# Optimization experiments

Measured on AMD Instinct MI355X. Metric: run time of the kernel, lower is better.

The kernel has to match this reference:

```python
import jax, jax.numpy as jnp
import numpy as np

C = 256
CQK = C // 8  # query/key channel dim from Conv3d(in, in//8, 1)


def setup_inputs() -> dict:
    key = jax.random.key(0)
    ks = jax.random.split(key, 8)
    B, D, H, W = 2, 16, 16, 16
    x = jax.random.normal(ks[0], (B, C, D, H, W), dtype=jnp.float32)
    s = 1.0 / np.sqrt(C)
    q_w = jax.random.normal(ks[1], (CQK, C), dtype=jnp.float32) * s
    q_b = jax.random.normal(ks[2], (CQK,), dtype=jnp.float32) * 0.01
    k_w = jax.random.normal(ks[3], (CQK, C), dtype=jnp.float32) * s
    k_b = jax.random.normal(ks[4], (CQK,), dtype=jnp.float32) * 0.01
    v_w = jax.random.normal(ks[5], (C, C), dtype=jnp.float32) * s
    v_b = jax.random.normal(ks[6], (C,), dtype=jnp.float32) * 0.01
    gamma = jax.random.normal(ks[7], (1,), dtype=jnp.float32)
    return {"x": x, "q_w": q_w, "q_b": q_b, "k_w": k_w, "k_b": k_b,
            "v_w": v_w, "v_b": v_b, "gamma": gamma}


def reference(x, q_w, q_b, k_w, k_b, v_w, v_b, gamma):
    B, Cc, D, H, W = x.shape
    N = D * H * W
    xf = x.reshape(B, Cc, N)  # [B, C, N]
    # 1x1x1 Conv3d == channel-mixing matmul
    q = jnp.einsum('oc,bcn->bon', q_w, xf) + q_b[None, :, None]  # [B, C/8, N]
    k = jnp.einsum('oc,bcn->bon', k_w, xf) + k_b[None, :, None]  # [B, C/8, N]
    v = jnp.einsum('oc,bcn->bon', v_w, xf) + v_b[None, :, None]  # [B, C, N]
    # attention[b, i, j] = sum_c q[b, c, i] * k[b, c, j]
    attn = jnp.einsum('bci,bcj->bij', q, k)  # [B, N, N]
    attn = jax.nn.softmax(attn, axis=-1)
    # out[b, c, i] = sum_j v[b, c, j] * attn[b, i, j]
    out = jnp.einsum('bcj,bij->bci', v, attn)  # [B, C, N]
    out = out.reshape(B, Cc, D, H, W)
    return gamma[0] * out + x
```

## Files before the change

kernel.cpp:

```cpp
#include <hip/hip_runtime.h>

#define C_DIM 256
#define CQK   32
#define N_DIM 4096
#define B_DIM 2

typedef __attribute__((ext_vector_type(8))) short bf16x8;
typedef __attribute__((ext_vector_type(4))) float f32x4;

__device__ __forceinline__ unsigned short f2bf(float f) {
    union { float f; unsigned u; } v; v.f = f;
    unsigned r = v.u + 0x7FFFu + ((v.u >> 16) & 1u);
    return (unsigned short)(r >> 16);
}
__device__ __forceinline__ unsigned pk2(float a, float b) {
    return (unsigned)f2bf(a) | ((unsigned)f2bf(b) << 16);
}
__device__ __forceinline__ unsigned pk2t(float a, float b) {
    union { float f; unsigned u; } ua, ub; ua.f = a; ub.f = b;
    return __builtin_amdgcn_perm(ub.u, ua.u, 0x07060302u);
}
#define EXP2(x) __builtin_amdgcn_exp2f(x)
#define MFMA(A, B, C) __builtin_amdgcn_mfma_f32_16x16x32_bf16((A), (B), (C), 0, 0, 0)

__global__ __launch_bounds__(256) void wconv(
    const float* __restrict__ q_w, const float* __restrict__ q_b,
    const float* __restrict__ k_w, const float* __restrict__ k_b,
    const float* __restrict__ v_w, const float* __restrict__ v_b,
    unsigned short* __restrict__ wbf, float* __restrict__ biasf)
{
    const float LOG2E = 1.4426950408889634f;
    int o = blockIdx.x, c = threadIdx.x;
    float w;
    if (o < 32)       w = q_w[o * C_DIM + c] * LOG2E;
    else if (o < 64)  w = k_w[(o - 32) * C_DIM + c];
    else              w = v_w[(o - 64) * C_DIM + c];
    wbf[o * C_DIM + c] = f2bf(w);
    if (c == 0) biasf[o] = (o < 32) ? q_b[o] * LOG2E
                         : (o < 64) ? k_b[o - 32] : v_b[o - 64];
}

__global__ __launch_bounds__(256, 2) void qkv_proj(
    const float* __restrict__ x, const unsigned short* __restrict__ wbf,
    const float* __restrict__ biasf,
    unsigned short* __restrict__ qT, unsigned short* __restrict__ kT,
    unsigned short* __restrict__ vbf)
{
    __shared__ __align__(16) unsigned short xsT[32 * 264];
    __shared__ __align__(16) unsigned short qkbuf[2][32 * 36];
    __shared__ __align__(16) unsigned short vbb[256 * 36];
    const int t  = threadIdx.x;
    const int b  = blockIdx.x >> 7;
    const int n0 = (blockIdx.x & 127) * 32;

    {
        int n4 = t & 3, cq = t >> 2;
        const float* xp = x + ((size_t)(b * C_DIM + cq * 4)) * N_DIM + n0 + n4 * 8;
        float a0[8], a1[8], a2[8], a3[8];
        *(float4*)(a0)     = *(const float4*)(xp);
        *(float4*)(a0 + 4) = *(const float4*)(xp + 4);
        *(float4*)(a1)     = *(const float4*)(xp + N_DIM);
        *(float4*)(a1 + 4) = *(const float4*)(xp + N_DIM + 4);
        *(float4*)(a2)     = *(const float4*)(xp + 2 * N_DIM);
        *(float4*)(a2 + 4) = *(const float4*)(xp + 2 * N_DIM + 4);
        *(float4*)(a3)     = *(const float4*)(xp + 3 * N_DIM);
        *(float4*)(a3 + 4) = *(const float4*)(xp + 3 * N_DIM + 4);
        #pragma unroll
        for (int k = 0; k < 8; ++k) {
            uint2 pw;
            pw.x = pk2(a0[k], a1[k]);
            pw.y = pk2(a2[k], a3[k]);
            *(uint2*)&xsT[(n4 * 8 + k) * 264 + cq * 4] = pw;
        }
    }
    __syncthreads();

    const int w = t >> 6, lid = t & 63, lr = lid & 15, lq = lid >> 4;
    f32x4 acc[5][2] = {};
    #pragma unroll
    for (int ks = 0; ks < 8; ++ks) {
        bf16x8 xb0 = *(const bf16x8*)&xsT[lr * 264 + ks * 32 + lq * 8];
        bf16x8 xb1 = *(const bf16x8*)&xsT[(16 + lr) * 264 + ks * 32 + lq * 8];
        #pragma unroll
        for (int u = 0; u < 5; ++u) {
            int gm = w * 5 + u;
            bf16x8 af = *(const bf16x8*)&wbf[(gm * 16 + lr) * C_DIM + ks * 32 + lq * 8];
            acc[u][0] = MFMA(af, xb0, acc[u][0]);
            acc[u][1] = MFMA(af, xb1, acc[u][1]);
        }
    }
    #pragma unroll
    for (int u = 0; u < 5; ++u) {
        int gm = w * 5 + u;
        float bv[4];
        *(float4*)bv = *(const float4*)&biasf[gm * 16 + lq * 4];
        #pragma unroll
        for (int nh = 0; nh < 2; ++nh) {
            if (gm >= 4) {
                int vc = (gm - 4) * 16 + lq * 4;
                #pragma unroll
                for (int r = 0; r < 4; ++r)
                    vbb[(vc + r) * 36 + nh * 16 + lr] = f2bf(acc[u][nh][r] + bv[r]);
            } else {
                int sel = gm >> 1, half = gm & 1;
                uint2 pw;
                pw.x = pk2(acc[u][nh][0] + bv[0], acc[u][nh][1] + bv[1]);
                pw.y = pk2(acc[u][nh][2] + bv[2], acc[u][nh][3] + bv[3]);
                *(uint2*)&qkbuf[sel][(nh * 16 + lr) * 36 + half * 16 + lq * 4] = pw;
            }
        }
    }
    __syncthreads();
    {
        int sel = t >> 7, idx = t & 127;
        int n = idx >> 2, ch8 = (idx & 3) * 8;
        const unsigned short* src = &qkbuf[sel][n * 36 + ch8];
        uint2 a = *(const uint2*)src;
        uint2 c = *(const uint2*)(src + 4);
        unsigned short* dst = (sel ? kT : qT) + ((size_t)b * N_DIM + n0 + n) * CQK + ch8;
        uint4 st; st.x = a.x; st.y = a.y; st.z = c.x; st.w = c.y;
        *(uint4*)dst = st;
    }
    {
        const unsigned short* src = &vbb[t * 36];
        uint2 a = *(const uint2*)(src + 0);
        uint2 bq = *(const uint2*)(src + 4);
        uint2 c = *(const uint2*)(src + 8);
        uint2 d = *(const uint2*)(src + 12);
        uint2 e = *(const uint2*)(src + 16);
        uint2 f = *(const uint2*)(src + 20);
        uint2 g = *(const uint2*)(src + 24);
        uint2 h = *(const uint2*)(src + 28);
        unsigned short* dst = vbf +
            (((size_t)(b * 4 + (t >> 6)) * 128 + (n0 >> 5)) * 64 + (t & 63)) * 32;
        uint4 s0; s0.x = a.x; s0.y = a.y; s0.z = bq.x; s0.w = bq.y;
        uint4 s1; s1.x = c.x; s1.y = c.y; s1.z = d.x; s1.w = d.y;
        uint4 s2; s2.x = e.x; s2.y = e.y; s2.z = f.x; s2.w = f.y;
        uint4 s3; s3.x = g.x; s3.y = g.y; s3.z = h.x; s3.w = h.y;
        *(uint4*)(dst)      = s0;
        *(uint4*)(dst + 8)  = s1;
        *(uint4*)(dst + 16) = s2;
        *(uint4*)(dst + 24) = s3;
    }
}

__global__ __launch_bounds__(256, 2) void attn_kernel(
    const unsigned short* __restrict__ qT, const unsigned short* __restrict__ kT,
    const unsigned short* __restrict__ vbf, const float* __restrict__ x,
    const float* __restrict__ gamma, float* __restrict__ out)
{
    __shared__ __align__(16) char smem[40960 + 1536];
    unsigned short* pbase = (unsigned short*)smem;
    float* obuf = (float*)smem;
    float* lbuf = (float*)(smem + 40960);

    const int t  = threadIdx.x;
    const int b  = blockIdx.x >> 8;
    const int qt = (blockIdx.x >> 2) & 63;
    const int cs = blockIdx.x & 3;
    const int i0 = qt * 64;
    const int w = t >> 6, lid = t & 63, lr = lid & 15, lq = lid >> 4;

    const unsigned short* qTb = qT + (size_t)b * N_DIM * CQK;
    const unsigned short* kTb = kT + (size_t)b * N_DIM * CQK;
    const unsigned short* vtb = vbf + (size_t)(b * 4 + cs) * 128 * 2048;

    unsigned short* pW0 = pbase + (w * 2 + 0) * (64 * 40);
    unsigned short* pW1 = pbase + (w * 2 + 1) * (64 * 40);

    bf16x8 bq[4];
    #pragma unroll
    for (int it = 0; it < 4; ++it)
        bq[it] = *(const bf16x8*)&qTb[(i0 + it * 16 + lr) * CQK + lq * 8];

    f32x4 oa[4][4] = {};
    float lp[4] = {};

    const int jwbase = w * 1024;
    const int vlane = lr * 32 + lq * 8;

    bf16x8 akc0 = *(const bf16x8*)&kTb[(jwbase + lr) * CQK + lq * 8];
    bf16x8 akc1 = *(const bf16x8*)&kTb[(jwbase + 16 + lr) * CQK + lq * 8];
    bf16x8 avU[4];

    {
        const unsigned short* vt0 = vtb + (size_t)(w * 32) * 2048;
        #pragma unroll
        for (int ct = 0; ct < 4; ++ct)
            avU[ct] = *(const bf16x8*)&vt0[ct * 512 + vlane];
        bf16x8 akn0 = *(const bf16x8*)&kTb[(jwbase + 32 + lr) * CQK + lq * 8];
        bf16x8 akn1 = *(const bf16x8*)&kTb[(jwbase + 32 + 16 + lr) * CQK + lq * 8];
        const f32x4 z = {};
        #pragma unroll
        for (int it = 0; it < 4; ++it) {
            f32x4 s0 = MFMA(akc0, bq[it], z);
            f32x4 s1 = MFMA(akc1, bq[it], z);
            float e0 = EXP2(s0[0]), e1 = EXP2(s0[1]), e2 = EXP2(s0[2]), e3 = EXP2(s0[3]);
            float f0 = EXP2(s1[0]), f1 = EXP2(s1[1]), f2 = EXP2(s1[2]), f3 = EXP2(s1[3]);
            lp[it] += ((e0 + e1) + (e2 + e3)) + ((f0 + f1) + (f2 + f3));
            uint2 pw0; pw0.x = pk2t(e0, e1); pw0.y = pk2t(e2, e3);
            uint2 pw1; pw1.x = pk2t(f0, f1); pw1.y = pk2t(f2, f3);
            unsigned short* prow = pW0 + (it * 16 + lr) * 40;
            *(uint2*)&prow[lq * 4]      = pw0;
            *(uint2*)&prow[16 + lq * 4] = pw1;
        }
        akc0 = akn0; akc1 = akn1;
    }

    #pragma unroll 2
    for (int k = 1; k < 32; ++k) {
        const int jn = jwbase + ((k + 1) & 31) * 32;
        const unsigned short* vtk = vtb + (size_t)(w * 32 + k) * 2048;
        bf16x8 avI[4];
        #pragma unroll
        for (int ct = 0; ct < 4; ++ct)
            avI[ct] = *(const bf16x8*)&vtk[ct * 512 + vlane];
        bf16x8 akn0 = *(const bf16x8*)&kTb[(jn + lr) * CQK + lq * 8];
        bf16x8 akn1 = *(const bf16x8*)&kTb[(jn + 16 + lr) * CQK + lq * 8];
        const unsigned short* pR = (k & 1) ? pW0 : pW1;
        bf16x8 bp[4];
        #pragma unroll
        for (int it = 0; it < 4; ++it)
            bp[it] = *(const bf16x8*)&pR[(it * 16 + lr) * 40 + lq * 8];
        const f32x4 z = {};
        f32x4 s[4][2];
        #pragma unroll
        for (int it = 0; it < 4; ++it) {
            s[it][0] = MFMA(akc0, bq[it], z);
            s[it][1] = MFMA(akc1, bq[it], z);
        }
        #pragma unroll
        for (int it = 0; it < 4; ++it)
            #pragma unroll
            for (int ct = 0; ct < 4; ++ct)
                oa[ct][it] = MFMA(avU[ct], bp[it], oa[ct][it]);
        unsigned short* pWc = (k & 1) ? pW1 : pW0;
        #pragma unroll
        for (int it = 0; it < 4; ++it) {
            float e0 = EXP2(s[it][0][0]), e1 = EXP2(s[it][0][1]);
            float e2 = EXP2(s[it][0][2]), e3 = EXP2(s[it][0][3]);
            float f0 = EXP2(s[it][1][0]), f1 = EXP2(s[it][1][1]);
            float f2 = EXP2(s[it][1][2]), f3 = EXP2(s[it][1][3]);
            lp[it] += ((e0 + e1) + (e2 + e3)) + ((f0 + f1) + (f2 + f3));
            uint2 pw0; pw0.x = pk2t(e0, e1); pw0.y = pk2t(e2, e3);
            uint2 pw1; pw1.x = pk2t(f0, f1); pw1.y = pk2t(f2, f3);
            unsigned short* prow = pWc + (it * 16 + lr) * 40;
            *(uint2*)&prow[lq * 4]      = pw0;
            *(uint2*)&prow[16 + lq * 4] = pw1;
        }
        akc0 = akn0; akc1 = akn1;
        #pragma unroll
        for (int ct = 0; ct < 4; ++ct) avU[ct] = avI[ct];
    }

    {
        bf16x8 bp[4];
        #pragma unroll
        for (int it = 0; it < 4; ++it)
            bp[it] = *(const bf16x8*)&pW1[(it * 16 + lr) * 40 + lq * 8];
        #pragma unroll
        for (int it = 0; it < 4; ++it)
            #pragma unroll
            for (int ct = 0; ct < 4; ++ct)
                oa[ct][it] = MFMA(avU[ct], bp[it], oa[ct][it]);
    }

    #pragma unroll
    for (int it = 0; it < 4; ++it) {
        lp[it] += __shfl_xor(lp[it], 16);
        lp[it] += __shfl_xor(lp[it], 32);
    }
    if (lq == 0) {
        #pragma unroll
        for (int it = 0; it < 4; ++it)
            lbuf[w * 64 + it * 16 + lr] = lp[it];
    }
    __syncthreads();

    for (int ph = 0; ph < 4; ++ph) {
        if (w == ph) {
            #pragma unroll
            for (int ct = 0; ct < 4; ++ct)
                #pragma unroll
                for (int it = 0; it < 4; ++it)
                    #pragma unroll
                    for (int r = 0; r < 4; ++r) {
                        int addr = (ct * 16 + lq * 4 + r) * 68 + it * 16 + lr;
                        if (ph == 0) obuf[addr]  = oa[ct][it][r];
                        else         obuf[addr] += oa[ct][it][r];
                    }
        }
        __syncthreads();
    }
    if (t < 64) {
        float l = lbuf[t] + lbuf[64 + t] + lbuf[128 + t] + lbuf[192 + t];
        lbuf[256 + t] = 1.f / l;
    }
    __syncthreads();

    const float g2 = gamma[0];
    const int c0 = cs * 64;
    const int cc = t >> 2;
    const int ic = (t & 3) * 16;
    const size_t rowbase = ((size_t)b * C_DIM + c0 + cc) * N_DIM + i0 + ic;
    #pragma unroll
    for (int k = 0; k < 4; ++k) {
        float4 ov4 = *(const float4*)&obuf[cc * 68 + ic + k * 4];
        float4 li  = *(const float4*)&lbuf[256 + ic + k * 4];
        float4 xv  = *(const float4*)(x + rowbase + k * 4);
        float4 ov;
        ov.x = g2 * ov4.x * li.x + xv.x;
        ov.y = g2 * ov4.y * li.y + xv.y;
        ov.z = g2 * ov4.z * li.z + xv.z;
        ov.w = g2 * ov4.w * li.w + xv.w;
        *(float4*)(out + rowbase + k * 4) = ov;
    }
}

extern "C" void kernel_launch(void* const* d_in, const int* in_sizes, int n_in,
                              void* d_out, int out_size, void* d_ws, size_t ws_size,
                              hipStream_t stream) {
    const float* x     = (const float*)d_in[0];
    const float* q_w   = (const float*)d_in[1];
    const float* q_b   = (const float*)d_in[2];
    const float* k_w   = (const float*)d_in[3];
    const float* k_b   = (const float*)d_in[4];
    const float* v_w   = (const float*)d_in[5];
    const float* v_b   = (const float*)d_in[6];
    const float* gamma = (const float*)d_in[7];
    float* out = (float*)d_out;

    char* ws = (char*)d_ws;
    unsigned short* qT    = (unsigned short*)(ws);
    unsigned short* kT    = (unsigned short*)(ws + 524288);
    unsigned short* vbf   = (unsigned short*)(ws + 1048576);
    unsigned short* wbf   = (unsigned short*)(ws + 5242880);
    float*          biasf = (float*)(ws + 5406720);

    hipLaunchKernelGGL(wconv, dim3(320), dim3(256), 0, stream,
                       q_w, q_b, k_w, k_b, v_w, v_b, wbf, biasf);
    hipLaunchKernelGGL(qkv_proj, dim3(B_DIM * 128), dim3(256), 0, stream,
                       x, wbf, biasf, qT, kT, vbf);
    hipLaunchKernelGGL(attn_kernel, dim3(B_DIM * 64 * 4), dim3(256), 0, stream,
                       qT, kT, vbf, x, gamma, out);
}
```

Before: 120.4 us.

## Split attention by query rows per wave instead of key ranges, drop LDS reduction

Each wave now owns 16 query rows and walks all 4096 keys, instead of four waves splitting the key range for 64 shared rows. The cross-wave LDS reduction of output and row sums, plus its barriers, is removed, and results are written straight from registers. Blocks grow to 512 threads covering 128 queries, and the grid halves. In exchange each wave issues fewer MFMAs per K/V load, so K and V fetches are reused less. The epilogue also uses scalar, less coalesced global stores.

```diff
diff --git a/kernel.cpp b/kernel.cpp
--- a/kernel.cpp
+++ b/kernel.cpp
@@ -144,73 +144,63 @@
     }
 }
 
-__global__ __launch_bounds__(256, 2) void attn_kernel(
+__global__ __launch_bounds__(512, 2) void attn_kernel(
     const unsigned short* __restrict__ qT, const unsigned short* __restrict__ kT,
     const unsigned short* __restrict__ vbf, const float* __restrict__ x,
     const float* __restrict__ gamma, float* __restrict__ out)
 {
-    __shared__ __align__(16) char smem[40960 + 1536];
-    unsigned short* pbase = (unsigned short*)smem;
-    float* obuf = (float*)smem;
-    float* lbuf = (float*)(smem + 40960);
+    __shared__ __align__(16) unsigned short pbase[8 * 2 * 640];
 
     const int t  = threadIdx.x;
-    const int b  = blockIdx.x >> 8;
-    const int qt = (blockIdx.x >> 2) & 63;
+    const int b  = blockIdx.x >> 7;
+    const int qt = (blockIdx.x >> 2) & 31;
     const int cs = blockIdx.x & 3;
-    const int i0 = qt * 64;
+    const int i0 = qt * 128;
+    const int c0 = cs * 64;
     const int w = t >> 6, lid = t & 63, lr = lid & 15, lq = lid >> 4;
 
     const unsigned short* qTb = qT + (size_t)b * N_DIM * CQK;
     const unsigned short* kTb = kT + (size_t)b * N_DIM * CQK;
     const unsigned short* vtb = vbf + (size_t)(b * 4 + cs) * 128 * 2048;
 
-    unsigned short* pW0 = pbase + (w * 2 + 0) * (64 * 40);
-    unsigned short* pW1 = pbase + (w * 2 + 1) * (64 * 40);
-
-    bf16x8 bq[4];
-    #pragma unroll
-    for (int it = 0; it < 4; ++it)
-        bq[it] = *(const bf16x8*)&qTb[(i0 + it * 16 + lr) * CQK + lq * 8];
-
-    f32x4 oa[4][4] = {};
-    float lp[4] = {};
-
-    const int jwbase = w * 1024;
+    unsigned short* pW0 = pbase + (w * 2 + 0) * 640;
+    unsigned short* pW1 = pbase + (w * 2 + 1) * 640;
+
+    bf16x8 bq = *(const bf16x8*)&qTb[(i0 + w * 16 + lr) * CQK + lq * 8];
+
+    f32x4 oa[4] = {};
+    float lp = 0.f;
+
     const int vlane = lr * 32 + lq * 8;
 
-    bf16x8 akc0 = *(const bf16x8*)&kTb[(jwbase + lr) * CQK + lq * 8];
-    bf16x8 akc1 = *(const bf16x8*)&kTb[(jwbase + 16 + lr) * CQK + lq * 8];
+    bf16x8 akc0 = *(const bf16x8*)&kTb[(lr) * CQK + lq * 8];
+    bf16x8 akc1 = *(const bf16x8*)&kTb[(16 + lr) * CQK + lq * 8];
     bf16x8 avU[4];
 
     {
-        const unsigned short* vt0 = vtb + (size_t)(w * 32) * 2048;
-        #pragma unroll
-        for (int ct = 0; ct < 4; ++ct)
-            avU[ct] = *(const bf16x8*)&vt0[ct * 512 + vlane];
-        bf16x8 akn0 = *(const bf16x8*)&kTb[(jwbase + 32 + lr) * CQK + lq * 8];
-        bf16x8 akn1 = *(const bf16x8*)&kTb[(jwbase + 32 + 16 + lr) * CQK + lq * 8];
+        #pragma unroll
+        for (int ct = 0; ct < 4; ++ct)
+            avU[ct] = *(const bf16x8*)&vtb[ct * 512 + vlane];
+        bf16x8 akn0 = *(const bf16x8*)&kTb[(32 + lr) * CQK + lq * 8];
+        bf16x8 akn1 = *(const bf16x8*)&kTb[(32 + 16 + lr) * CQK + lq * 8];
         const f32x4 z = {};
-        #pragma unroll
-        for (int it = 0; it < 4; ++it) {
-            f32x4 s0 = MFMA(akc0, bq[it], z);
-            f32x4 s1 = MFMA(akc1, bq[it], z);
-            float e0 = EXP2(s0[0]), e1 = EXP2(s0[1]), e2 = EXP2(s0[2]), e3 = EXP2(s0[3]);
-            float f0 = EXP2(s1[0]), f1 = EXP2(s1[1]), f2 = EXP2(s1[2]), f3 = EXP2(s1[3]);
-            lp[it] += ((e0 + e1) + (e2 + e3)) + ((f0 + f1) + (f2 + f3));
-            uint2 pw0; pw0.x = pk2t(e0, e1); pw0.y = pk2t(e2, e3);
-            uint2 pw1; pw1.x = pk2t(f0, f1); pw1.y = pk2t(f2, f3);
-            unsigned short* prow = pW0 + (it * 16 + lr) * 40;
-            *(uint2*)&prow[lq * 4]      = pw0;
-            *(uint2*)&prow[16 + lq * 4] = pw1;
-        }
+        f32x4 s0 = MFMA(akc0, bq, z);
+        f32x4 s1 = MFMA(akc1, bq, z);
+        float e0 = EXP2(s0[0]), e1 = EXP2(s0[1]), e2 = EXP2(s0[2]), e3 = EXP2(s0[3]);
+        float f0 = EXP2(s1[0]), f1 = EXP2(s1[1]), f2 = EXP2(s1[2]), f3 = EXP2(s1[3]);
+        lp += ((e0 + e1) + (e2 + e3)) + ((f0 + f1) + (f2 + f3));
+        uint2 pw0; pw0.x = pk2t(e0, e1); pw0.y = pk2t(e2, e3);
+        uint2 pw1; pw1.x = pk2t(f0, f1); pw1.y = pk2t(f2, f3);
+        unsigned short* prow = pW0 + lr * 40;
+        *(uint2*)&prow[lq * 4]      = pw0;
+        *(uint2*)&prow[16 + lq * 4] = pw1;
         akc0 = akn0; akc1 = akn1;
     }
 
     #pragma unroll 2
-    for (int k = 1; k < 32; ++k) {
-        const int jn = jwbase + ((k + 1) & 31) * 32;
-        const unsigned short* vtk = vtb + (size_t)(w * 32 + k) * 2048;
+    for (int k = 1; k < 128; ++k) {
+        const int jn = ((k + 1) & 127) * 32;
+        const unsigned short* vtk = vtb + (size_t)k * 2048;
         bf16x8 avI[4];
         #pragma unroll
         for (int ct = 0; ct < 4; ++ct)
@@ -218,102 +208,47 @@
         bf16x8 akn0 = *(const bf16x8*)&kTb[(jn + lr) * CQK + lq * 8];
         bf16x8 akn1 = *(const bf16x8*)&kTb[(jn + 16 + lr) * CQK + lq * 8];
         const unsigned short* pR = (k & 1) ? pW0 : pW1;
-        bf16x8 bp[4];
-        #pragma unroll
-        for (int it = 0; it < 4; ++it)
-            bp[it] = *(const bf16x8*)&pR[(it * 16 + lr) * 40 + lq * 8];
+        bf16x8 bp = *(const bf16x8*)&pR[lr * 40 + lq * 8];
         const f32x4 z = {};
-        f32x4 s[4][2];
-        #pragma unroll
-        for (int it = 0; it < 4; ++it) {
-            s[it][0] = MFMA(akc0, bq[it], z);
-            s[it][1] = MFMA(akc1, bq[it], z);
-        }
-        #pragma unroll
-        for (int it = 0; it < 4; ++it)
-            #pragma unroll
-            for (int ct = 0; ct < 4; ++ct)
-                oa[ct][it] = MFMA(avU[ct], bp[it], oa[ct][it]);
+        f32x4 s0 = MFMA(akc0, bq, z);
+        f32x4 s1 = MFMA(akc1, bq, z);
+        #pragma unroll
+        for (int ct = 0; ct < 4; ++ct)
+            oa[ct] = MFMA(avU[ct], bp, oa[ct]);
+        float e0 = EXP2(s0[0]), e1 = EXP2(s0[1]), e2 = EXP2(s0[2]), e3 = EXP2(s0[3]);
+        float f0 = EXP2(s1[0]), f1 = EXP2(s1[1]), f2 = EXP2(s1[2]), f3 = EXP2(s1[3]);
+        lp += ((e0 + e1) + (e2 + e3)) + ((f0 + f1) + (f2 + f3));
+        uint2 pw0; pw0.x = pk2t(e0, e1); pw0.y = pk2t(e2, e3);
+        uint2 pw1; pw1.x = pk2t(f0, f1); pw1.y = pk2t(f2, f3);
         unsigned short* pWc = (k & 1) ? pW1 : pW0;
-        #pragma unroll
-        for (int it = 0; it < 4; ++it) {
-            float e0 = EXP2(s[it][0][0]), e1 = EXP2(s[it][0][1]);
-            float e2 = EXP2(s[it][0][2]), e3 = EXP2(s[it][0][3]);
-            float f0 = EXP2(s[it][1][0]), f1 = EXP2(s[it][1][1]);
-            float f2 = EXP2(s[it][1][2]), f3 = EXP2(s[it][1][3]);
-            lp[it] += ((e0 + e1) + (e2 + e3)) + ((f0 + f1) + (f2 + f3));
-            uint2 pw0; pw0.x = pk2t(e0, e1); pw0.y = pk2t(e2, e3);
-            uint2 pw1; pw1.x = pk2t(f0, f1); pw1.y = pk2t(f2, f3);
-            unsigned short* prow = pWc + (it * 16 + lr) * 40;
-            *(uint2*)&prow[lq * 4]      = pw0;
-            *(uint2*)&prow[16 + lq * 4] = pw1;
-        }
+        unsigned short* prow = pWc + lr * 40;
+        *(uint2*)&prow[lq * 4]      = pw0;
+        *(uint2*)&prow[16 + lq * 4] = pw1;
         akc0 = akn0; akc1 = akn1;
         #pragma unroll
         for (int ct = 0; ct < 4; ++ct) avU[ct] = avI[ct];
     }
 
     {
-        bf16x8 bp[4];
-        #pragma unroll
-        for (int it = 0; it < 4; ++it)
-            bp[it] = *(const bf16x8*)&pW1[(it * 16 + lr) * 40 + lq * 8];
-        #pragma unroll
-        for (int it = 0; it < 4; ++it)
-            #pragma unroll
-            for (int ct = 0; ct < 4; ++ct)
-                oa[ct][it] = MFMA(avU[ct], bp[it], oa[ct][it]);
-    }
-
+        bf16x8 bp = *(const bf16x8*)&pW1[lr * 40 + lq * 8];
+        #pragma unroll
+        for (int ct = 0; ct < 4; ++ct)
+            oa[ct] = MFMA(avU[ct], bp, oa[ct]);
+    }
+
+    lp += __shfl_xor(lp, 16);
+    lp += __shfl_xor(lp, 32);
+    const float linv = 1.f / lp;
+
+    const float gl = gamma[0];
     #pragma unroll
-    for (int it = 0; it < 4; ++it) {
-        lp[it] += __shfl_xor(lp[it], 16);
-        lp[it] += __shfl_xor(lp[it], 32);
-    }
-    if (lq == 0) {
-        #pragma unroll
-        for (int it = 0; it < 4; ++it)
-            lbuf[w * 64 + it * 16 + lr] = lp[it];
-    }
-    __syncthreads();
-
-    for (int ph = 0; ph < 4; ++ph) {
-        if (w == ph) {
-            #pragma unroll
-            for (int ct = 0; ct < 4; ++ct)
-                #pragma unroll
-                for (int it = 0; it < 4; ++it)
-                    #pragma unroll
-                    for (int r = 0; r < 4; ++r) {
-                        int addr = (ct * 16 + lq * 4 + r) * 68 + it * 16 + lr;
-                        if (ph == 0) obuf[addr]  = oa[ct][it][r];
-                        else         obuf[addr] += oa[ct][it][r];
-                    }
-        }
-        __syncthreads();
-    }
-    if (t < 64) {
-        float l = lbuf[t] + lbuf[64 + t] + lbuf[128 + t] + lbuf[192 + t];
-        lbuf[256 + t] = 1.f / l;
-    }
-    __syncthreads();
-
-    const float g2 = gamma[0];
-    const int c0 = cs * 64;
-    const int cc = t >> 2;
-    const int ic = (t & 3) * 16;
-    const size_t rowbase = ((size_t)b * C_DIM + c0 + cc) * N_DIM + i0 + ic;
-    #pragma unroll
-    for (int k = 0; k < 4; ++k) {
-        float4 ov4 = *(const float4*)&obuf[cc * 68 + ic + k * 4];
-        float4 li  = *(const float4*)&lbuf[256 + ic + k * 4];
-        float4 xv  = *(const float4*)(x + rowbase + k * 4);
-        float4 ov;
-        ov.x = g2 * ov4.x * li.x + xv.x;
-        ov.y = g2 * ov4.y * li.y + xv.y;
-        ov.z = g2 * ov4.z * li.z + xv.z;
-        ov.w = g2 * ov4.w * li.w + xv.w;
-        *(float4*)(out + rowbase + k * 4) = ov;
+    for (int ct = 0; ct < 4; ++ct) {
+        #pragma unroll
+        for (int r = 0; r < 4; ++r) {
+            int c = c0 + ct * 16 + lq * 4 + r;
+            size_t addr = ((size_t)(b * C_DIM + c)) * N_DIM + i0 + w * 16 + lr;
+            out[addr] = gl * oa[ct][r] * linv + x[addr];
+        }
     }
 }
 
@@ -341,6 +276,6 @@
                        q_w, q_b, k_w, k_b, v_w, v_b, wbf, biasf);
     hipLaunchKernelGGL(qkv_proj, dim3(B_DIM * 128), dim3(256), 0, stream,
                        x, wbf, biasf, qT, kT, vbf);
-    hipLaunchKernelGGL(attn_kernel, dim3(B_DIM * 64 * 4), dim3(256), 0, stream,
+    hipLaunchKernelGGL(attn_kernel, dim3(B_DIM * 32 * 4), dim3(512), 0, stream,
                        qT, kT, vbf, x, gamma, out);
 }
```

After: 176.2 us. 1.46x slower.
